# Kernel optimization log

Measured on AMD Instinct MI355X. Metric: run time of the kernel, lower is better.

Reference implementation:

```python
import jax, jax.numpy as jnp
import numpy as np

G = 60   # rotation group size
K = 13   # SO3 neighbors per group element


def data_process(x, nei):
    # x: [B, C, 60] -> gather neighbors -> [B, C, 60, 13]
    b, c = x.shape[0], x.shape[1]
    return x[:, :, nei].reshape(b, c, G, K)


def comb_conv(x4, W, b):
    # x4: [B, C, 60, 13], W: [O, C, 13] (Conv2d kernel (1,13) squeezed) -> [B, O, 60]
    return jnp.einsum('bcgk,ock->bog', x4, W) + b[None, :, None]


def bn_relu(x, gamma, beta):
    # eval-mode BatchNorm2d folded to per-channel affine, then ReLU
    return jax.nn.relu(x * gamma[None, :, None] + beta[None, :, None])


def group_feat_net(feats, nei, W_in, b_in, W1, b1, g1, be1, W2, b2, g2, be2, Wo, bo, go, beo):
    # Conv_in: plain conv, no BN/ReLU
    d = comb_conv(data_process(feats, nei), W_in, b_in)              # [B,256,60]
    # Residual_Comb_Conv(256,512,256)
    fc = bn_relu(comb_conv(data_process(d, nei), W1, b1), g1, be1)   # [B,512,60]
    fc = bn_relu(comb_conv(data_process(fc, nei), W2, b2), g2, be2)  # [B,256,60]
    d = d + fc
    # Conv_out = Comb_Conv(256,32)
    d = bn_relu(comb_conv(data_process(d, nei), Wo, bo), go, beo)    # [B,32,60]
    eqv = d + feats
    inv = jnp.mean(eqv, axis=-1)                                     # [B,32]
    eqv = eqv / jnp.maximum(jnp.linalg.norm(eqv, axis=1, keepdims=True), 1e-4)
    inv = inv / jnp.maximum(jnp.linalg.norm(inv, axis=1, keepdims=True), 1e-4)
    return inv, eqv


def des2dr(des1, des2, permu):
    # des1, des2: [B,32,60]; permu: [3600] -> gather -> [B,32,60,60]
    b, f = des1.shape[0], des1.shape[1]
    d1p = des1[:, :, permu].reshape(b, f, G, G)
    cor = jnp.einsum('bfag,bfg->ba', d1p, des2)                      # [B,60]
    return jnp.argmax(cor, axis=1)


def setup_inputs() -> dict:
    key = jax.random.key(0)
    ks = jax.random.split(key, 16)
    B = 256
    inp = {
        'feats0': jax.random.normal(ks[0], (B, 32, G), dtype=jnp.float32),
        'feats1': jax.random.normal(ks[1], (B, 32, G), dtype=jnp.float32),
        'true_idx': jax.random.randint(ks[2], (B,), 0, G, dtype=jnp.int32),
        'nei_idx': jax.random.randint(ks[3], (G * K,), 0, G, dtype=jnp.int32),
        'permu_idx': jax.random.randint(ks[4], (G * G,), 0, G, dtype=jnp.int32),
        'W_in': jax.random.normal(ks[5], (256, 32, K), dtype=jnp.float32) * 0.05,
        'b_in': jnp.zeros((256,), dtype=jnp.float32),
        'W1': jax.random.normal(ks[6], (512, 256, K), dtype=jnp.float32) * 0.02,
        'b1': jnp.zeros((512,), dtype=jnp.float32),
        'g1': jnp.ones((512,), dtype=jnp.float32),
        'be1': jnp.zeros((512,), dtype=jnp.float32),
        'W2': jax.random.normal(ks[7], (256, 512, K), dtype=jnp.float32) * 0.02,
        'b2': jnp.zeros((256,), dtype=jnp.float32),
        'g2': jnp.ones((256,), dtype=jnp.float32),
        'be2': jnp.zeros((256,), dtype=jnp.float32),
        'Wo': jax.random.normal(ks[8], (32, 256, K), dtype=jnp.float32) * 0.02,
        'bo': jnp.zeros((32,), dtype=jnp.float32),
        'go': jnp.ones((32,), dtype=jnp.float32),
        'beo': jnp.zeros((32,), dtype=jnp.float32),
    }
    return inp


def reference(feats0, feats1, true_idx, nei_idx, permu_idx,
              W_in, b_in, W1, b1, g1, be1, W2, b2, g2, be2, Wo, bo, go, beo):
    params = (W_in, b_in, W1, b1, g1, be1, W2, b2, g2, be2, Wo, bo, go, beo)
    inv0, eqv0 = group_feat_net(feats0, nei_idx, *params)
    inv1, eqv1 = group_feat_net(feats1, nei_idx, *params)
    pre_idxs = des2dr(eqv0, eqv1, permu_idx)
    ability = jnp.mean((pre_idxs == true_idx).astype(jnp.float32))
    return (feats0, feats1, eqv0, eqv1, inv0, inv1, ability, true_idx, pre_idxs)
```

## Files before the change

kernel.cpp:

```cpp
#include <hip/hip_runtime.h>

#define G60 60
#define KN 13

typedef unsigned int u32;
typedef unsigned short u16;
typedef short short8 __attribute__((ext_vector_type(8)));
typedef float f32x4 __attribute__((ext_vector_type(4)));
typedef float f32x16 __attribute__((ext_vector_type(16)));
typedef u32 u32x4 __attribute__((ext_vector_type(4)));

template <int I> struct Ic { static constexpr int v = I; };
template <int I, int N, typename F>
__device__ __forceinline__ void sfor(F&& f) {
    if constexpr (I < N) { f(Ic<I>{}); sfor<I + 1, N>(f); }
}

__device__ __forceinline__ u32 f32_to_packed(float v) {
    u32 u = __float_as_uint(v);
    u32 hi = (u + 0x7FFFu + ((u >> 16) & 1u)) >> 16;
    float vhi = __uint_as_float(hi << 16);
    float lof = v - vhi;
    u32 ul = __float_as_uint(lof);
    u32 lo = (ul + 0x7FFFu + ((ul >> 16) & 1u)) >> 16;
    return (hi << 16) | lo;
}
__device__ __forceinline__ float packed_f32(u32 w) {
    return __uint_as_float(w & 0xFFFF0000u) + __uint_as_float(w << 16);
}

__device__ __forceinline__ void pack_one(const float* __restrict__ W,
                                         u16* __restrict__ Whi, u16* __restrict__ Wlo,
                                         int C, int O, int CT, int id) {
    int j = id & 7;
    int lane = (id >> 3) & 63;
    int fid = id >> 9;
    int NTt = O >> 5;
    int nt = fid % NTt;
    int t = fid / NTt;
    int SUBS = CT >> 4;
    int sub = t % SUBS;
    int kk = (t / SUBS) % KN;
    int ct = t / (KN * SUBS);
    int q = lane >> 5, n = lane & 31;
    int o = nt * 32 + n;
    int c = ct * CT + sub * 16 + q * 8 + j;
    u32 pw = f32_to_packed(W[((size_t)o * C + c) * KN + kk]);
    Whi[id] = (u16)(pw >> 16);
    Wlo[id] = (u16)(pw & 0xFFFFu);
}

__global__ void __launch_bounds__(256) pack_all_kern(
    const float* W_in, u16* Whi_in, u16* Wlo_in,
    const float* W1, u16* Whi_1, u16* Wlo_1,
    const float* W2, u16* Whi_2, u16* Wlo_2,
    const float* Wo, u16* Whi_o, u16* Wlo_o) {
    const int T0 = KN * 32 * 256;
    const int T1 = T0 + KN * 256 * 512;
    const int T2 = T1 + KN * 512 * 256;
    const int T3 = T2 + KN * 256 * 32;
    int id = blockIdx.x * 256 + threadIdx.x;
    if (id < T0) pack_one(W_in, Whi_in, Wlo_in, 32, 256, 32, id);
    else if (id < T1) pack_one(W1, Whi_1, Wlo_1, 256, 512, 64, id - T0);
    else if (id < T2) pack_one(W2, Whi_2, Wlo_2, 512, 256, 64, id - T1);
    else if (id < T3) pack_one(Wo, Whi_o, Wlo_o, 256, 32, 64, id - T2);
}

template <int CT, int NB, int NTB, int NWN, int SRC, bool BNR, bool OUTF32>
__global__ void __launch_bounds__(NWN * 64, 2) mconv6(
    const u32* __restrict__ Xp, const float* __restrict__ Xf,
    const float* __restrict__ pIn,
    const float* __restrict__ bnb, const float* __restrict__ bng,
    const float* __restrict__ bnB,
    const u32* __restrict__ resid,
    const u16* __restrict__ Whi, const u16* __restrict__ Wlo,
    const float* __restrict__ bias, const float* __restrict__ gamma,
    const float* __restrict__ beta,
    const int* __restrict__ nei,
    u32* __restrict__ outp, float* __restrict__ outf,
    int C, int O, int tpz) {
    constexpr int SUBS = CT >> 4;
    constexpr int S = KN * SUBS;
    constexpr int NG = S / 2;
    constexpr int STRIDE = CT + 8;
    constexpr int PLSZ = G60 * STRIDE;
    constexpr int THREADS = NWN * 64;
    __shared__ u16 Xs[NB * 2 * PLSZ];
    const int tid = threadIdx.x;
    const int lane = tid & 63;
    const int wv = tid >> 6;
    const int q = lane >> 5;
    const int m = lane & 31;
    const int bp = blockIdx.x;
    const int NTt = O >> 5;
    const int nt0 = ((int)blockIdx.y * NWN + wv) * NTB;
    const int ct0 = (int)blockIdx.z * tpz;
    const size_t PLi = (size_t)256 * C * G60;
    float* outfz = OUTF32 ? (outf + (size_t)blockIdx.z * ((size_t)256 * O * G60)) : nullptr;

    int rowoff[2][KN];
#pragma unroll
    for (int mt = 0; mt < 2; ++mt) {
        int g = mt * 32 + m;
        int gl = (g < G60) ? g : 0;
#pragma unroll
        for (int kk = 0; kk < KN; ++kk) rowoff[mt][kk] = nei[gl * KN + kk] * STRIDE;
    }

    f32x16 acc[NB][2][NTB];
#pragma unroll
    for (int bb = 0; bb < NB; ++bb)
#pragma unroll
        for (int mt = 0; mt < 2; ++mt)
#pragma unroll
            for (int nt = 0; nt < NTB; ++nt) acc[bb][mt][nt] = (f32x16)(0.f);

    short8 Bh[2][2][NTB], Bl[2][2][NTB];

    for (int ct = ct0; ct < ct0 + tpz; ++ct) {
        const size_t fbase = ((size_t)(ct * S) * NTt + nt0) * 512 + (size_t)lane * 8;

        __syncthreads();
        constexpr int PAIRS = (CT / 2) * G60;
        for (int i = tid; i < NB * PAIRS; i += THREADS) {
            int bb = (NB == 2 && i >= PAIRS) ? 1 : 0;
            int r = i - bb * PAIRS;
            int ccp = (r * 17477) >> 20;
            int g = r - ccp * G60;
            int cc = ccp * 2;
            size_t cg0 = ((size_t)(bp * NB + bb) * C + (size_t)ct * CT + cc) * G60 + g;
            u32 w0, w1;
            if (SRC == 0) {
                w0 = Xp[cg0]; w1 = Xp[cg0 + G60];
            } else if (SRC == 1) {
                w0 = f32_to_packed(Xf[cg0]); w1 = f32_to_packed(Xf[cg0 + G60]);
            } else {
                int c0 = ct * CT + cc;
                float v0 = pIn[cg0] + pIn[PLi + cg0];
                float v1 = pIn[cg0 + G60] + pIn[PLi + cg0 + G60];
                v0 = fmaxf((v0 + bnb[c0]) * bng[c0] + bnB[c0], 0.f) + packed_f32(resid[cg0]);
                v1 = fmaxf((v1 + bnb[c0 + 1]) * bng[c0 + 1] + bnB[c0 + 1], 0.f) + packed_f32(resid[cg0 + G60]);
                w0 = f32_to_packed(v0); w1 = f32_to_packed(v1);
            }
            int rb = bb * 2 * PLSZ + g * STRIDE + cc;
            *(u32*)(Xs + rb) = (w0 >> 16) | (w1 & 0xFFFF0000u);
            *(u32*)(Xs + rb + PLSZ) = (w0 & 0xFFFFu) | (w1 << 16);
        }

        sfor<0, 2>([&](auto uc) {
            constexpr int u = decltype(uc)::v;
            sfor<0, NTB>([&](auto nc) {
                constexpr int nt = decltype(nc)::v;
                const size_t fb = fbase + ((size_t)u * NTt + nt) * 512;
                Bh[0][u][nt] = *reinterpret_cast<const short8*>(Whi + fb);
                Bl[0][u][nt] = *reinterpret_cast<const short8*>(Wlo + fb);
            });
        });
        __syncthreads();

        sfor<0, NG>([&](auto gc) {
            constexpr int g = decltype(gc)::v;
            constexpr int pb = g & 1;
            if constexpr (g + 1 < NG) {
                constexpr int pn = (g + 1) & 1;
                sfor<0, 2>([&](auto uc) {
                    constexpr int u = decltype(uc)::v;
                    constexpr int s = 2 * (g + 1) + u;
                    sfor<0, NTB>([&](auto nc) {
                        constexpr int nt = decltype(nc)::v;
                        const size_t fb = fbase + ((size_t)s * NTt + nt) * 512;
                        Bh[pn][u][nt] = *reinterpret_cast<const short8*>(Whi + fb);
                        Bl[pn][u][nt] = *reinterpret_cast<const short8*>(Wlo + fb);
                    });
                });
            }
            short8 Ah[2][NB][2], Al[2][NB][2];
            sfor<0, 2>([&](auto uc) {
                constexpr int u = decltype(uc)::v;
                constexpr int s = 2 * g + u;
                constexpr int kk = s / SUBS;
                constexpr int sub = s - kk * SUBS;
                sfor<0, NB>([&](auto bc) {
                    constexpr int bb = decltype(bc)::v;
                    sfor<0, 2>([&](auto mc) {
                        constexpr int mt = decltype(mc)::v;
                        const int off = bb * 2 * PLSZ + rowoff[mt][kk] + sub * 16 + q * 8;
                        Ah[u][bb][mt] = *reinterpret_cast<const short8*>(Xs + off);
                        Al[u][bb][mt] = *reinterpret_cast<const short8*>(Xs + off + PLSZ);
                    });
                });
            });
            sfor<0, 2>([&](auto uc) {
                constexpr int u = decltype(uc)::v;
                sfor<0, NTB>([&](auto nc) {
                    constexpr int nt = decltype(nc)::v;
                    sfor<0, NB>([&](auto bc) {
                        constexpr int bb = decltype(bc)::v;
                        sfor<0, 2>([&](auto mc) {
                            constexpr int mt = decltype(mc)::v;
                            acc[bb][mt][nt] = __builtin_amdgcn_mfma_f32_32x32x16_bf16(
                                Ah[u][bb][mt], Bh[pb][u][nt], acc[bb][mt][nt], 0, 0, 0);
                        });
                    });
                });
                sfor<0, NTB>([&](auto nc) {
                    constexpr int nt = decltype(nc)::v;
                    sfor<0, NB>([&](auto bc) {
                        constexpr int bb = decltype(bc)::v;
                        sfor<0, 2>([&](auto mc) {
                            constexpr int mt = decltype(mc)::v;
                            acc[bb][mt][nt] = __builtin_amdgcn_mfma_f32_32x32x16_bf16(
                                Ah[u][bb][mt], Bl[pb][u][nt], acc[bb][mt][nt], 0, 0, 0);
                        });
                    });
                });
                sfor<0, NTB>([&](auto nc) {
                    constexpr int nt = decltype(nc)::v;
                    sfor<0, NB>([&](auto bc) {
                        constexpr int bb = decltype(bc)::v;
                        sfor<0, 2>([&](auto mc) {
                            constexpr int mt = decltype(mc)::v;
                            acc[bb][mt][nt] = __builtin_amdgcn_mfma_f32_32x32x16_bf16(
                                Al[u][bb][mt], Bh[pb][u][nt], acc[bb][mt][nt], 0, 0, 0);
                        });
                    });
                });
            });
        });
    }

#pragma unroll
    for (int nt = 0; nt < NTB; ++nt) {
        const int o = (nt0 + nt) * 32 + m;
        float bi = 0.f, ga = 1.f, be = 0.f;
        if (!OUTF32) { bi = bias[o]; if (BNR) { ga = gamma[o]; be = beta[o]; } }
#pragma unroll
        for (int bb = 0; bb < NB; ++bb) {
            const int b = bp * NB + bb;
#pragma unroll
            for (int mt = 0; mt < 2; ++mt) {
#pragma unroll
                for (int grp = 0; grp < 4; ++grp) {
                    const int g0 = mt * 32 + grp * 8 + q * 4;
                    if (g0 < G60) {
                        size_t oi = ((size_t)b * O + o) * G60 + g0;
                        if (OUTF32) {
                            f32x4 v;
#pragma unroll
                            for (int rr = 0; rr < 4; ++rr) v[rr] = acc[bb][mt][nt][grp * 4 + rr];
                            *reinterpret_cast<f32x4*>(outfz + oi) = v;
                        } else {
                            u32x4 pv;
#pragma unroll
                            for (int rr = 0; rr < 4; ++rr) {
                                float v = acc[bb][mt][nt][grp * 4 + rr] + bi;
                                if (BNR) v = fmaxf(v * ga + be, 0.f);
                                pv[rr] = f32_to_packed(v);
                            }
                            *reinterpret_cast<u32x4*>(outp + oi) = pv;
                        }
                    }
                }
            }
        }
    }
}

__global__ void __launch_bounds__(64) finalize_kern(
    const float* __restrict__ pout,
    const float* __restrict__ feats,
    const float* __restrict__ bo, const float* __restrict__ go,
    const float* __restrict__ beo,
    float* __restrict__ out_feats,
    float* __restrict__ out_eqv,
    float* __restrict__ out_inv) {
    const int b = blockIdx.x;
    const size_t PB = (size_t)256 * 32 * G60;
    __shared__ float E[32 * G60];
    __shared__ float gnorm[G60];
    __shared__ float inv_pre[32];
    __shared__ float inv_nrm;
    const int tid = threadIdx.x;

    for (int i = tid; i < 32 * G60; i += 64) {
        int f = i / G60;
        size_t idx = (size_t)b * 1920 + i;
        float ft = feats[idx];
        out_feats[idx] = ft;
        float s = pout[idx] + pout[PB + idx] + pout[2 * PB + idx] + pout[3 * PB + idx];
        float v = fmaxf((s + bo[f]) * go[f] + beo[f], 0.f);
        E[i] = v + ft;
    }
    __syncthreads();
    if (tid < G60) {
        float s = 0.f;
        for (int f = 0; f < 32; ++f) { float v = E[f * G60 + tid]; s += v * v; }
        gnorm[tid] = fmaxf(sqrtf(s), 1e-4f);
    }
    if (tid < 32) {
        float s = 0.f;
        for (int g = 0; g < G60; ++g) s += E[tid * G60 + g];
        inv_pre[tid] = s / 60.f;
    }
    __syncthreads();
    if (tid == 0) {
        float s = 0.f;
        for (int f = 0; f < 32; ++f) s += inv_pre[f] * inv_pre[f];
        inv_nrm = fmaxf(sqrtf(s), 1e-4f);
    }
    __syncthreads();
    for (int i = tid; i < 1920; i += 64) {
        int g = i % G60;
        out_eqv[(size_t)b * 1920 + i] = E[i] / gnorm[g];
    }
    if (tid < 32) out_inv[b * 32 + tid] = inv_pre[tid] / inv_nrm;
}

__global__ void __launch_bounds__(256) des2dr_kern(
    const float* __restrict__ e0f, const float* __restrict__ e1f,
    const int* __restrict__ permu, int* __restrict__ pre_int,
    float* __restrict__ out_pre) {
    const int b = blockIdx.x;
    __shared__ float X0[32 * G60];
    __shared__ float X1[32 * G60];
    __shared__ float pc[256];
    __shared__ float cor[64];
    const int tid = threadIdx.x;
    for (int i = tid; i < 1920; i += 256) {
        X0[i] = e0f[(size_t)b * 1920 + i];
        X1[i] = e1f[(size_t)b * 1920 + i];
    }
    __syncthreads();
    const int a = tid >> 2, fc = tid & 3;
    float s = 0.f;
    if (a < G60) {
        for (int g = 0; g < G60; ++g) {
            int p = permu[a * G60 + g];
#pragma unroll
            for (int f = fc * 8; f < fc * 8 + 8; ++f) s += X0[f * G60 + p] * X1[f * G60 + g];
        }
    }
    pc[tid] = s;
    __syncthreads();
    if (tid < 64) cor[tid] = pc[4 * tid] + pc[4 * tid + 1] + pc[4 * tid + 2] + pc[4 * tid + 3];
    __syncthreads();
    if (tid == 0) {
        float best = cor[0];
        int bi = 0;
        for (int a2 = 1; a2 < G60; ++a2)
            if (cor[a2] > best) { best = cor[a2]; bi = a2; }
        pre_int[b] = bi;
        out_pre[b] = (float)bi;
    }
}

__global__ void __launch_bounds__(256) ability_kern(
    const int* __restrict__ pre_int, const int* __restrict__ true_idx,
    float* __restrict__ out_ability, float* __restrict__ out_true) {
    __shared__ int cnt[256];
    const int t = threadIdx.x;
    cnt[t] = (pre_int[t] == true_idx[t]) ? 1 : 0;
    out_true[t] = (float)true_idx[t];
    __syncthreads();
    for (int s = 128; s > 0; s >>= 1) {
        if (t < s) cnt[t] += cnt[t + s];
        __syncthreads();
    }
    if (t == 0) out_ability[0] = (float)cnt[0] / 256.0f;
}

extern "C" void kernel_launch(void* const* d_in, const int* in_sizes, int n_in,
                              void* d_out, int out_size, void* d_ws, size_t ws_size,
                              hipStream_t stream) {
    const float* feats0 = (const float*)d_in[0];
    const float* feats1 = (const float*)d_in[1];
    const int* true_idx = (const int*)d_in[2];
    const int* nei = (const int*)d_in[3];
    const int* permu = (const int*)d_in[4];
    const float* W_in = (const float*)d_in[5];
    const float* b_in = (const float*)d_in[6];
    const float* W1 = (const float*)d_in[7];
    const float* b1 = (const float*)d_in[8];
    const float* g1 = (const float*)d_in[9];
    const float* be1 = (const float*)d_in[10];
    const float* W2 = (const float*)d_in[11];
    const float* b2 = (const float*)d_in[12];
    const float* g2 = (const float*)d_in[13];
    const float* be2 = (const float*)d_in[14];
    const float* Wo = (const float*)d_in[15];
    const float* bo = (const float*)d_in[16];
    const float* go = (const float*)d_in[17];
    const float* beo = (const float*)d_in[18];

    float* out = (float*)d_out;
    const size_t SZF = (size_t)256 * 32 * G60;
    float* out_f0 = out;
    float* out_f1 = out + SZF;
    float* out_e0 = out + 2 * SZF;
    float* out_e1 = out + 3 * SZF;
    float* out_i0 = out + 4 * SZF;
    float* out_i1 = out_i0 + 256 * 32;
    float* out_ab = out_i1 + 256 * 32;
    float* out_tr = out_ab + 1;
    float* out_pr = out_tr + 256;

    char* p = (char*)d_ws;
    auto alloc = [&](size_t bytes) { char* r = p; p += (bytes + 255) & ~(size_t)255; return r; };
    const size_t NW_IN = (size_t)KN * 32 * 256;
    const size_t NW_1 = (size_t)KN * 256 * 512;
    const size_t NW_2 = (size_t)KN * 512 * 256;
    const size_t NW_O = (size_t)KN * 256 * 32;
    u16* Whi_in = (u16*)alloc(NW_IN * 2); u16* Wlo_in = (u16*)alloc(NW_IN * 2);
    u16* Whi_1 = (u16*)alloc(NW_1 * 2);   u16* Wlo_1 = (u16*)alloc(NW_1 * 2);
    u16* Whi_2 = (u16*)alloc(NW_2 * 2);   u16* Wlo_2 = (u16*)alloc(NW_2 * 2);
    u16* Whi_o = (u16*)alloc(NW_O * 2);   u16* Wlo_o = (u16*)alloc(NW_O * 2);
    u32* dbuf = (u32*)alloc((size_t)256 * 256 * G60 * 4);
    u32* fcbuf = (u32*)alloc((size_t)256 * 512 * G60 * 4);
    float* p2 = (float*)alloc((size_t)2 * 256 * 256 * G60 * 4);
    float* pout = (float*)alloc((size_t)4 * SZF * 4);
    int* pre_int = (int*)alloc(256 * 4);

    {
        int total = KN * (32 * 256 + 256 * 512 + 512 * 256 + 256 * 32);
        pack_all_kern<<<dim3((total + 255) / 256), dim3(256), 0, stream>>>(
            W_in, Whi_in, Wlo_in, W1, Whi_1, Wlo_1, W2, Whi_2, Wlo_2, Wo, Whi_o, Wlo_o);
    }

    for (int net = 0; net < 2; ++net) {
        const float* feats = net ? feats1 : feats0;
        float* of = net ? out_f1 : out_f0;
        float* oe = net ? out_e1 : out_e0;
        float* oi = net ? out_i1 : out_i0;

        mconv6<32, 1, 1, 4, 1, false, false><<<dim3(256, 2, 1), dim3(256), 0, stream>>>(
            nullptr, feats, nullptr, nullptr, nullptr, nullptr, nullptr,
            Whi_in, Wlo_in, b_in, nullptr, nullptr, nei, dbuf, nullptr, 32, 256, 1);
        mconv6<64, 2, 1, 4, 0, true, false><<<dim3(128, 4, 1), dim3(256), 0, stream>>>(
            dbuf, nullptr, nullptr, nullptr, nullptr, nullptr, nullptr,
            Whi_1, Wlo_1, b1, g1, be1, nei, fcbuf, nullptr, 256, 512, 4);
        mconv6<64, 2, 1, 4, 0, false, true><<<dim3(128, 2, 2), dim3(256), 0, stream>>>(
            fcbuf, nullptr, nullptr, nullptr, nullptr, nullptr, nullptr,
            Whi_2, Wlo_2, nullptr, nullptr, nullptr, nei, nullptr, p2, 512, 256, 4);
        mconv6<64, 2, 1, 1, 2, false, true><<<dim3(128, 1, 4), dim3(64), 0, stream>>>(
            nullptr, nullptr, p2, b2, g2, be2, dbuf,
            Whi_o, Wlo_o, nullptr, nullptr, nullptr, nei, nullptr, pout, 256, 32, 1);
        finalize_kern<<<dim3(256), dim3(64), 0, stream>>>(pout, feats, bo, go, beo, of, oe, oi);
    }

    des2dr_kern<<<dim3(256), dim3(256), 0, stream>>>(out_e0, out_e1, permu, pre_int, out_pr);
    ability_kern<<<dim3(1), dim3(256), 0, stream>>>(pre_int, true_idx, out_ab, out_tr);

    (void)in_sizes; (void)n_in; (void)out_size; (void)ws_size;
}
```

Before: 826.7 us.

## Split MFMA conv waves over batch and row tiles, each wave covering several output tiles

```diff
diff --git a/kernel.cpp b/kernel.cpp
--- a/kernel.cpp
+++ b/kernel.cpp
@@ -66,8 +66,8 @@
     else if (id < T3) pack_one(Wo, Whi_o, Wlo_o, 256, 32, 64, id - T2);
 }
 
-template <int CT, int NB, int NTB, int NWN, int SRC, bool BNR, bool OUTF32>
-__global__ void __launch_bounds__(NWN * 64, 2) mconv6(
+template <int CT, int NTB, int SRC, bool BNR, bool OUTF32>
+__global__ void __launch_bounds__(256, 2) mconv7(
     const u32* __restrict__ Xp, const float* __restrict__ Xf,
     const float* __restrict__ pIn,
     const float* __restrict__ bnb, const float* __restrict__ bng,
@@ -84,36 +84,33 @@
     constexpr int NG = S / 2;
     constexpr int STRIDE = CT + 8;
     constexpr int PLSZ = G60 * STRIDE;
-    constexpr int THREADS = NWN * 64;
-    __shared__ u16 Xs[NB * 2 * PLSZ];
+    __shared__ u16 Xs[4 * PLSZ];
     const int tid = threadIdx.x;
     const int lane = tid & 63;
     const int wv = tid >> 6;
+    const int bb = wv & 1;
+    const int mt = wv >> 1;
     const int q = lane >> 5;
     const int m = lane & 31;
     const int bp = blockIdx.x;
     const int NTt = O >> 5;
-    const int nt0 = ((int)blockIdx.y * NWN + wv) * NTB;
+    const int nt0 = (int)blockIdx.y * NTB;
     const int ct0 = (int)blockIdx.z * tpz;
     const size_t PLi = (size_t)256 * C * G60;
     float* outfz = OUTF32 ? (outf + (size_t)blockIdx.z * ((size_t)256 * O * G60)) : nullptr;
 
-    int rowoff[2][KN];
-#pragma unroll
-    for (int mt = 0; mt < 2; ++mt) {
+    int rowoff[KN];
+    {
         int g = mt * 32 + m;
         int gl = (g < G60) ? g : 0;
 #pragma unroll
-        for (int kk = 0; kk < KN; ++kk) rowoff[mt][kk] = nei[gl * KN + kk] * STRIDE;
-    }
-
-    f32x16 acc[NB][2][NTB];
-#pragma unroll
-    for (int bb = 0; bb < NB; ++bb)
-#pragma unroll
-        for (int mt = 0; mt < 2; ++mt)
-#pragma unroll
-            for (int nt = 0; nt < NTB; ++nt) acc[bb][mt][nt] = (f32x16)(0.f);
+        for (int kk = 0; kk < KN; ++kk)
+            rowoff[kk] = nei[gl * KN + kk] * STRIDE + bb * 2 * PLSZ;
+    }
+
+    f32x16 acc[NTB];
+#pragma unroll
+    for (int nt = 0; nt < NTB; ++nt) acc[nt] = (f32x16)(0.f);
 
     short8 Bh[2][2][NTB], Bl[2][2][NTB];
 
@@ -122,13 +119,13 @@
 
         __syncthreads();
         constexpr int PAIRS = (CT / 2) * G60;
-        for (int i = tid; i < NB * PAIRS; i += THREADS) {
-            int bb = (NB == 2 && i >= PAIRS) ? 1 : 0;
-            int r = i - bb * PAIRS;
+        for (int i = tid; i < 2 * PAIRS; i += 256) {
+            int sb = (i >= PAIRS) ? 1 : 0;
+            int r = i - sb * PAIRS;
             int ccp = (r * 17477) >> 20;
             int g = r - ccp * G60;
             int cc = ccp * 2;
-            size_t cg0 = ((size_t)(bp * NB + bb) * C + (size_t)ct * CT + cc) * G60 + g;
+            size_t cg0 = ((size_t)(bp * 2 + sb) * C + (size_t)ct * CT + cc) * G60 + g;
             u32 w0, w1;
             if (SRC == 0) {
                 w0 = Xp[cg0]; w1 = Xp[cg0 + G60];
@@ -142,7 +139,7 @@
                 v1 = fmaxf((v1 + bnb[c0 + 1]) * bng[c0 + 1] + bnB[c0 + 1], 0.f) + packed_f32(resid[cg0 + G60]);
                 w0 = f32_to_packed(v0); w1 = f32_to_packed(v1);
             }
-            int rb = bb * 2 * PLSZ + g * STRIDE + cc;
+            int rb = sb * 2 * PLSZ + g * STRIDE + cc;
             *(u32*)(Xs + rb) = (w0 >> 16) | (w1 & 0xFFFF0000u);
             *(u32*)(Xs + rb + PLSZ) = (w0 & 0xFFFFu) | (w1 << 16);
         }
@@ -174,92 +171,62 @@
                     });
                 });
             }
-            short8 Ah[2][NB][2], Al[2][NB][2];
+            short8 Ah[2], Al[2];
             sfor<0, 2>([&](auto uc) {
                 constexpr int u = decltype(uc)::v;
                 constexpr int s = 2 * g + u;
                 constexpr int kk = s / SUBS;
                 constexpr int sub = s - kk * SUBS;
-                sfor<0, NB>([&](auto bc) {
-                    constexpr int bb = decltype(bc)::v;
-                    sfor<0, 2>([&](auto mc) {
-                        constexpr int mt = decltype(mc)::v;
-                        const int off = bb * 2 * PLSZ + rowoff[mt][kk] + sub * 16 + q * 8;
-                        Ah[u][bb][mt] = *reinterpret_cast<const short8*>(Xs + off);
-                        Al[u][bb][mt] = *reinterpret_cast<const short8*>(Xs + off + PLSZ);
-                    });
-                });
+                const int off = rowoff[kk] + sub * 16 + q * 8;
+                Ah[u] = *reinterpret_cast<const short8*>(Xs + off);
+                Al[u] = *reinterpret_cast<const short8*>(Xs + off + PLSZ);
             });
             sfor<0, 2>([&](auto uc) {
                 constexpr int u = decltype(uc)::v;
                 sfor<0, NTB>([&](auto nc) {
                     constexpr int nt = decltype(nc)::v;
-                    sfor<0, NB>([&](auto bc) {
-                        constexpr int bb = decltype(bc)::v;
-                        sfor<0, 2>([&](auto mc) {
-                            constexpr int mt = decltype(mc)::v;
-                            acc[bb][mt][nt] = __builtin_amdgcn_mfma_f32_32x32x16_bf16(
-                                Ah[u][bb][mt], Bh[pb][u][nt], acc[bb][mt][nt], 0, 0, 0);
-                        });
-                    });
+                    acc[nt] = __builtin_amdgcn_mfma_f32_32x32x16_bf16(
+                        Ah[u], Bh[pb][u][nt], acc[nt], 0, 0, 0);
                 });
                 sfor<0, NTB>([&](auto nc) {
                     constexpr int nt = decltype(nc)::v;
-                    sfor<0, NB>([&](auto bc) {
-                        constexpr int bb = decltype(bc)::v;
-                        sfor<0, 2>([&](auto mc) {
-                            constexpr int mt = decltype(mc)::v;
-                            acc[bb][mt][nt] = __builtin_amdgcn_mfma_f32_32x32x16_bf16(
-                                Ah[u][bb][mt], Bl[pb][u][nt], acc[bb][mt][nt], 0, 0, 0);
-                        });
-                    });
+                    acc[nt] = __builtin_amdgcn_mfma_f32_32x32x16_bf16(
+                        Ah[u], Bl[pb][u][nt], acc[nt], 0, 0, 0);
                 });
                 sfor<0, NTB>([&](auto nc) {
                     constexpr int nt = decltype(nc)::v;
-                    sfor<0, NB>([&](auto bc) {
-                        constexpr int bb = decltype(bc)::v;
-                        sfor<0, 2>([&](auto mc) {
-                            constexpr int mt = decltype(mc)::v;
-                            acc[bb][mt][nt] = __builtin_amdgcn_mfma_f32_32x32x16_bf16(
-                                Al[u][bb][mt], Bh[pb][u][nt], acc[bb][mt][nt], 0, 0, 0);
-                        });
-                    });
+                    acc[nt] = __builtin_amdgcn_mfma_f32_32x32x16_bf16(
+                        Al[u], Bh[pb][u][nt], acc[nt], 0, 0, 0);
                 });
             });
         });
     }
 
+    const int b = bp * 2 + bb;
 #pragma unroll
     for (int nt = 0; nt < NTB; ++nt) {
         const int o = (nt0 + nt) * 32 + m;
         float bi = 0.f, ga = 1.f, be = 0.f;
         if (!OUTF32) { bi = bias[o]; if (BNR) { ga = gamma[o]; be = beta[o]; } }
 #pragma unroll
-        for (int bb = 0; bb < NB; ++bb) {
-            const int b = bp * NB + bb;
-#pragma unroll
-            for (int mt = 0; mt < 2; ++mt) {
-#pragma unroll
-                for (int grp = 0; grp < 4; ++grp) {
-                    const int g0 = mt * 32 + grp * 8 + q * 4;
-                    if (g0 < G60) {
-                        size_t oi = ((size_t)b * O + o) * G60 + g0;
-                        if (OUTF32) {
-                            f32x4 v;
-#pragma unroll
-                            for (int rr = 0; rr < 4; ++rr) v[rr] = acc[bb][mt][nt][grp * 4 + rr];
-                            *reinterpret_cast<f32x4*>(outfz + oi) = v;
-                        } else {
-                            u32x4 pv;
-#pragma unroll
-                            for (int rr = 0; rr < 4; ++rr) {
-                                float v = acc[bb][mt][nt][grp * 4 + rr] + bi;
-                                if (BNR) v = fmaxf(v * ga + be, 0.f);
-                                pv[rr] = f32_to_packed(v);
-                            }
-                            *reinterpret_cast<u32x4*>(outp + oi) = pv;
-                        }
+        for (int grp = 0; grp < 4; ++grp) {
+            const int g0 = mt * 32 + grp * 8 + q * 4;
+            if (g0 < G60) {
+                size_t oi = ((size_t)b * O + o) * G60 + g0;
+                if (OUTF32) {
+                    f32x4 v;
+#pragma unroll
+                    for (int rr = 0; rr < 4; ++rr) v[rr] = acc[nt][grp * 4 + rr];
+                    *reinterpret_cast<f32x4*>(outfz + oi) = v;
+                } else {
+                    u32x4 pv;
+#pragma unroll
+                    for (int rr = 0; rr < 4; ++rr) {
+                        float v = acc[nt][grp * 4 + rr] + bi;
+                        if (BNR) v = fmaxf(v * ga + be, 0.f);
+                        pv[rr] = f32_to_packed(v);
                     }
+                    *reinterpret_cast<u32x4*>(outp + oi) = pv;
                 }
             }
         }
@@ -432,16 +399,16 @@
         float* oe = net ? out_e1 : out_e0;
         float* oi = net ? out_i1 : out_i0;
 
-        mconv6<32, 1, 1, 4, 1, false, false><<<dim3(256, 2, 1), dim3(256), 0, stream>>>(
+        mconv7<32, 4, 1, false, false><<<dim3(128, 2, 1), dim3(256), 0, stream>>>(
             nullptr, feats, nullptr, nullptr, nullptr, nullptr, nullptr,
             Whi_in, Wlo_in, b_in, nullptr, nullptr, nei, dbuf, nullptr, 32, 256, 1);
-        mconv6<64, 2, 1, 4, 0, true, false><<<dim3(128, 4, 1), dim3(256), 0, stream>>>(
+        mconv7<64, 4, 0, true, false><<<dim3(128, 4, 1), dim3(256), 0, stream>>>(
             dbuf, nullptr, nullptr, nullptr, nullptr, nullptr, nullptr,
             Whi_1, Wlo_1, b1, g1, be1, nei, fcbuf, nullptr, 256, 512, 4);
-        mconv6<64, 2, 1, 4, 0, false, true><<<dim3(128, 2, 2), dim3(256), 0, stream>>>(
+        mconv7<64, 4, 0, false, true><<<dim3(128, 2, 2), dim3(256), 0, stream>>>(
             fcbuf, nullptr, nullptr, nullptr, nullptr, nullptr, nullptr,
             Whi_2, Wlo_2, nullptr, nullptr, nullptr, nei, nullptr, p2, 512, 256, 4);
-        mconv6<64, 2, 1, 1, 2, false, true><<<dim3(128, 1, 4), dim3(64), 0, stream>>>(
+        mconv7<64, 1, 2, false, true><<<dim3(128, 1, 4), dim3(256), 0, stream>>>(
             nullptr, nullptr, p2, b2, g2, be2, dbuf,
             Whi_o, Wlo_o, nullptr, nullptr, nullptr, nei, nullptr, pout, 256, 32, 1);
         finalize_kern<<<dim3(256), dim3(64), 0, stream>>>(pout, feats, bo, go, beo, of, oe, oi);
```

Measured after the change: 904.6 us. 9.4% more time.
